# Kernel tuning notes

Hardware: AMD Instinct MI355X
Metric: run time of the kernel (lower is better)

## Reference

```python
import jax, jax.numpy as jnp
import numpy as np

B, T, LD, HD, NH, NL = 8, 16, 256, 512, 8, 6
N = 65           # num_patches + 1 tokens per frame from encoder
AED = 64         # action_embed_dim
NDA = 11         # num_discrete_actions
MLP = 4 * HD


def _ln(x, g, b, eps=1e-5):
    m = jnp.mean(x, -1, keepdims=True)
    v = jnp.mean((x - m) ** 2, -1, keepdims=True)
    return (x - m) / jnp.sqrt(v + eps) * g + b


def setup_inputs() -> dict:
    key = jax.random.key(0)
    ks = iter(jax.random.split(key, 48))
    def nrm(shape):
        return jax.random.normal(next(ks), shape, jnp.float32) * 0.02
    inp = {
        'z_sequence': jax.random.normal(next(ks), (B, T, N, LD), jnp.float32),
        'continuous_actions': jax.random.normal(next(ks), (B, T, 2), jnp.float32),
        'discrete_actions': jax.random.randint(next(ks), (B, T), 0, NDA),
        'w_de': nrm((NDA, AED)),
        'w_cp': nrm((2, AED)), 'b_cp': jnp.zeros((AED,), jnp.float32),
        'w_ap': nrm((2 * AED, HD)), 'b_ap': jnp.zeros((HD,), jnp.float32),
        'w_tp': nrm((LD, HD)), 'b_tp': jnp.zeros((HD,), jnp.float32),
        'w_te': nrm((64, HD)),
        'ln1_g': jnp.ones((NL, HD), jnp.float32), 'ln1_b': jnp.zeros((NL, HD), jnp.float32),
        'wq': nrm((NL, HD, HD)), 'bq': jnp.zeros((NL, HD), jnp.float32),
        'wk': nrm((NL, HD, HD)), 'bk': jnp.zeros((NL, HD), jnp.float32),
        'wv': nrm((NL, HD, HD)), 'bv': jnp.zeros((NL, HD), jnp.float32),
        'wo': nrm((NL, HD, HD)), 'bo': jnp.zeros((NL, HD), jnp.float32),
        'ln2_g': jnp.ones((NL, HD), jnp.float32), 'ln2_b': jnp.zeros((NL, HD), jnp.float32),
        'w1': nrm((NL, HD, MLP)), 'b1': jnp.zeros((NL, MLP), jnp.float32),
        'w2': nrm((NL, MLP, HD)), 'b2': jnp.zeros((NL, HD), jnp.float32),
        'norm_g': jnp.ones((HD,), jnp.float32), 'norm_b': jnp.zeros((HD,), jnp.float32),
        'w_out': nrm((HD, LD)), 'b_out': jnp.zeros((LD,), jnp.float32),
        'residual_weight': jnp.float32(0.5),
    }
    return inp


def reference(z_sequence, continuous_actions, discrete_actions,
              w_de, w_cp, b_cp, w_ap, b_ap, w_tp, b_tp, w_te,
              ln1_g, ln1_b, wq, bq, wk, bk, wv, bv, wo, bo,
              ln2_g, ln2_b, w1, b1, w2, b2,
              norm_g, norm_b, w_out, b_out, residual_weight):
    Bq, Tq, Nq, Dq = z_sequence.shape
    hd = HD // NH
    scale = hd ** -0.5
    # --- per-timestep action + patch token embedding (vectorized over T) ---
    de = w_de[discrete_actions]                          # (B,T,AED)
    ce = continuous_actions @ w_cp + b_cp                # (B,T,AED)
    ac = jnp.concatenate([de, ce], -1)                   # (B,T,2*AED)
    at = (ac @ w_ap + b_ap)[:, :, None, :]               # (B,T,1,HD) action token
    pt = z_sequence @ w_tp + b_tp                        # (B,T,N,HD)
    te = w_te[:Tq][None, :, None, :]                     # (1,T,1,HD) time embedding
    x = jnp.concatenate([at + te, pt + te], axis=2)      # (B,T,1+N,HD) interleaved
    S = Tq * (Nq + 1)
    x = x.reshape(Bq, S, HD)
    # --- block-causal mask: True = cannot attend ---
    ts = jnp.repeat(jnp.arange(Tq), Nq + 1)
    mask = ts[None, :] > ts[:, None]                     # (S,S)

    def body(h, p):
        g1, be1, Wq, Bq_, Wk, Bk_, Wv, Bv_, Wo, Bo_, g2, be2, W1, B1, W2, B2 = p
        y = _ln(h, g1, be1)
        q = (y @ Wq + Bq_).reshape(Bq, S, NH, hd)
        k = (y @ Wk + Bk_).reshape(Bq, S, NH, hd)
        v = (y @ Wv + Bv_).reshape(Bq, S, NH, hd)
        sc = jnp.einsum('bqhd,bkhd->bhqk', q, k) * scale
        sc = jnp.where(mask[None, None], -jnp.inf, sc)
        a = jax.nn.softmax(sc, axis=-1)
        o = jnp.einsum('bhqk,bkhd->bqhd', a, v).reshape(Bq, S, HD)
        h = h + o @ Wo + Bo_
        y = _ln(h, g2, be2)
        h = h + jax.nn.gelu(y @ W1 + B1, approximate=False) @ W2 + B2
        return h, None

    x, _ = jax.lax.scan(body, x, (ln1_g, ln1_b, wq, bq, wk, bk, wv, bv, wo, bo,
                                  ln2_g, ln2_b, w1, b1, w2, b2))
    x = _ln(x, norm_g, norm_b)
    patch_out = x.reshape(Bq, Tq, Nq + 1, HD)[:, :, 1:, :] @ w_out + b_out
    alpha = jax.nn.sigmoid(residual_weight)
    return z_sequence + alpha * patch_out
```

## Files before the change

### kernel.cpp

```cpp
#include <hip/hip_runtime.h>
#include <hip/hip_bf16.h>
#include <cmath>

typedef __attribute__((ext_vector_type(8)))  __bf16 bf16x8;
typedef __attribute__((ext_vector_type(4)))  float  f32x4;
typedef __attribute__((ext_vector_type(16))) float  f32x16;
typedef const __attribute__((address_space(1))) void* as1cv;
typedef __attribute__((address_space(3))) void*       as3v;

static constexpr int BB = 8, TT = 16, NN = 65, LD = 256, HD = 512, NH = 8, NL = 6;
static constexpr int SS    = TT * (NN + 1);
static constexpr int ROWS  = BB * SS;
static constexpr int PROWS = BB * TT * NN;
static constexpr int MLPD  = 2048;

__global__ void transpose_cast(const float* __restrict__ in, __bf16* __restrict__ out,
                               int R, int C, size_t ibs, size_t obs)
{
  __shared__ float t[32][33];
  in  += ibs * blockIdx.z;
  out += obs * blockIdx.z;
  int bx = blockIdx.x * 32, by = blockIdx.y * 32;
  #pragma unroll
  for (int i = threadIdx.y; i < 32; i += 8)
    t[i][threadIdx.x] = in[(size_t)(by + i) * C + bx + threadIdx.x];
  __syncthreads();
  #pragma unroll
  for (int i = threadIdx.y; i < 32; i += 8)
    out[(size_t)(bx + i) * R + by + threadIdx.x] = (__bf16)t[threadIdx.x][i];
}

__global__ __launch_bounds__(256) void cast_bf16(const float* __restrict__ in,
                                                 __bf16* __restrict__ out)
{
  int i = (blockIdx.x * 256 + threadIdx.x) * 8;
  float4 a = *(const float4*)(in + i);
  float4 b = *(const float4*)(in + i + 4);
  bf16x8 o;
  o[0]=(__bf16)a.x; o[1]=(__bf16)a.y; o[2]=(__bf16)a.z; o[3]=(__bf16)a.w;
  o[4]=(__bf16)b.x; o[5]=(__bf16)b.y; o[6]=(__bf16)b.z; o[7]=(__bf16)b.w;
  *(bf16x8*)(out + i) = o;
}

__global__ void build_bqkv(const float* __restrict__ bq, const float* __restrict__ bk,
                           const float* __restrict__ bv, float* __restrict__ out)
{
  int i = blockIdx.x * 256 + threadIdx.x;
  int L = i / 1536, c = i % 1536;
  float v = (c < 512) ? bq[L*512 + c] : (c < 1024 ? bk[L*512 + c - 512] : bv[L*512 + c - 1024]);
  out[i] = v;
}

template<int FLAGS>
__global__ __launch_bounds__(256)
void gemm_bt(const __bf16* __restrict__ A, const __bf16* __restrict__ Bt,
             const float* __restrict__ bias, const float* __restrict__ resid,
             float* __restrict__ outF, __bf16* __restrict__ outB, __bf16* __restrict__ outB2,
             int M, int N, int K)
{
  __shared__ __bf16 As[128 * 64];
  __shared__ __bf16 Bs[128 * 64];
  const int tid = threadIdx.x;
  const int lane = tid & 63, w = tid >> 6;
  const int g = lane >> 4, cl = lane & 15;
  const int wr = w >> 1, wc = w & 1;
  const int tm = blockIdx.y * 128, tn = blockIdx.x * 128;

  f32x4 acc[4][4];
  const f32x4 zero4 = {0.f, 0.f, 0.f, 0.f};
  #pragma unroll
  for (int m = 0; m < 4; m++)
    #pragma unroll
    for (int n = 0; n < 4; n++) acc[m][n] = zero4;

  const int nk = K >> 6;
  for (int kt = 0; kt < nk; ++kt) {
    __syncthreads();
    const __bf16* Ag = A  + (size_t)tm * K + kt * 64;
    const __bf16* Bg = Bt + (size_t)tn * K + kt * 64;
    #pragma unroll
    for (int p = 0; p < 4; p++) {
      int c = p * 256 + tid;
      int row = c >> 3, j = c & 7;
      int jj = j ^ (row & 7);
      const __bf16* sa = Ag + (size_t)row * K + jj * 8;
      const __bf16* sb = Bg + (size_t)row * K + jj * 8;
      __bf16* la = &As[(p * 4 + w) * 512];
      __bf16* lb = &Bs[(p * 4 + w) * 512];
      __builtin_amdgcn_global_load_lds((as1cv)sa, (as3v)la, 16, 0, 0);
      __builtin_amdgcn_global_load_lds((as1cv)sb, (as3v)lb, 16, 0, 0);
    }
    __syncthreads();
    #pragma unroll
    for (int kk = 0; kk < 2; kk++) {
      bf16x8 af[4], bfr[4];
      #pragma unroll
      for (int m = 0; m < 4; m++) {
        int row = wr * 64 + m * 16 + cl;
        int j16 = (kk * 4 + g) ^ (row & 7);
        af[m] = *(const bf16x8*)&As[row * 64 + j16 * 8];
      }
      #pragma unroll
      for (int n = 0; n < 4; n++) {
        int row = wc * 64 + n * 16 + cl;
        int j16 = (kk * 4 + g) ^ (row & 7);
        bfr[n] = *(const bf16x8*)&Bs[row * 64 + j16 * 8];
      }
      #pragma unroll
      for (int m = 0; m < 4; m++)
        #pragma unroll
        for (int n = 0; n < 4; n++)
          acc[m][n] = __builtin_amdgcn_mfma_f32_16x16x32_bf16(af[m], bfr[n], acc[m][n], 0, 0, 0);
    }
  }
  float bv[4];
  #pragma unroll
  for (int n = 0; n < 4; n++) bv[n] = bias[tn + wc * 64 + n * 16 + cl];
  #pragma unroll
  for (int m = 0; m < 4; m++) {
    int Rb = tm + wr * 64 + m * 16 + g * 4;
    #pragma unroll
    for (int i = 0; i < 4; i++) {
      int R = Rb + i;
      #pragma unroll
      for (int n = 0; n < 4; n++) {
        int C = tn + wc * 64 + n * 16 + cl;
        float v = acc[m][n][i] + bv[n];
        if (FLAGS & 1) v = 0.5f * v * (1.f + erff(v * 0.70710678118f));
        if (FLAGS & 2) v += resid[(size_t)R * N + C];
        if (FLAGS & 8) outF[(size_t)R * N + C] = v;
        if (FLAGS & 4) outB[(size_t)R * N + C] = (__bf16)v;
        if (FLAGS & 32) {
          if (C < 1024) {
            outB[(size_t)R * 1024 + C] = (__bf16)v;
          } else {
            int bb2 = R / SS, s2 = R % SS;
            int cc = C - 1024, hh = cc >> 6, dd = cc & 63;
            outB2[((size_t)((bb2 * NH + hh) * 64 + dd)) * SS + s2] = (__bf16)v;
          }
        }
      }
    }
  }
}

__global__ __launch_bounds__(256) void ln_bf16(const float* __restrict__ in,
    const float* __restrict__ gam, const float* __restrict__ bet, __bf16* __restrict__ out)
{
  int w = threadIdx.x >> 6, l = threadIdx.x & 63;
  size_t row = (size_t)blockIdx.x * 4 + w;
  const float4* x4 = (const float4*)(in + row * HD);
  float4 v0 = x4[l], v1 = x4[l + 64];
  float s  = v0.x + v0.y + v0.z + v0.w + v1.x + v1.y + v1.z + v1.w;
  float q2 = v0.x*v0.x + v0.y*v0.y + v0.z*v0.z + v0.w*v0.w
           + v1.x*v1.x + v1.y*v1.y + v1.z*v1.z + v1.w*v1.w;
  #pragma unroll
  for (int m = 1; m < 64; m <<= 1) { s += __shfl_xor(s, m); q2 += __shfl_xor(q2, m); }
  float mean = s * (1.f / HD);
  float rstd = rsqrtf(q2 * (1.f / HD) - mean * mean + 1e-5f);
  int c0 = l * 4, c1 = 256 + l * 4;
  float4 g0 = *(const float4*)(gam + c0), g1 = *(const float4*)(gam + c1);
  float4 e0 = *(const float4*)(bet + c0), e1 = *(const float4*)(bet + c1);
  __bf16* o = out + row * HD;
  o[c0+0] = (__bf16)((v0.x-mean)*rstd*g0.x + e0.x);
  o[c0+1] = (__bf16)((v0.y-mean)*rstd*g0.y + e0.y);
  o[c0+2] = (__bf16)((v0.z-mean)*rstd*g0.z + e0.z);
  o[c0+3] = (__bf16)((v0.w-mean)*rstd*g0.w + e0.w);
  o[c1+0] = (__bf16)((v1.x-mean)*rstd*g1.x + e1.x);
  o[c1+1] = (__bf16)((v1.y-mean)*rstd*g1.y + e1.y);
  o[c1+2] = (__bf16)((v1.z-mean)*rstd*g1.z + e1.z);
  o[c1+3] = (__bf16)((v1.w-mean)*rstd*g1.w + e1.w);
}

__global__ __launch_bounds__(64) void act_embed(const float* __restrict__ cont,
    const int* __restrict__ disc, const float* __restrict__ w_de,
    const float* __restrict__ w_cp, const float* __restrict__ b_cp,
    const float* __restrict__ w_ap, const float* __restrict__ b_ap,
    const float* __restrict__ w_te, float* __restrict__ x)
{
  int t = blockIdx.x, b = blockIdx.y, l = threadIdx.x;
  int da = disc[b * TT + t];
  float c0 = cont[(b * TT + t) * 2], c1 = cont[(b * TT + t) * 2 + 1];
  int c = l * 8;
  float accv[8];
  #pragma unroll
  for (int j = 0; j < 8; j++) accv[j] = b_ap[c + j];
  for (int i = 0; i < 64; i++) {
    float ai = w_de[da * 64 + i];
    #pragma unroll
    for (int j = 0; j < 8; j++) accv[j] += ai * w_ap[i * HD + c + j];
  }
  for (int i = 0; i < 64; i++) {
    float ce = c0 * w_cp[i] + c1 * w_cp[64 + i] + b_cp[i];
    #pragma unroll
    for (int j = 0; j < 8; j++) accv[j] += ce * w_ap[(64 + i) * HD + c + j];
  }
  #pragma unroll
  for (int j = 0; j < 8; j++)
    x[((size_t)(b * SS) + t * 66) * HD + c + j] = accv[j] + w_te[t * HD + c + j];
}

__global__ __launch_bounds__(256) void assemble_patch(const float* __restrict__ pt,
    const float* __restrict__ te, float* __restrict__ x)
{
  int idx = (blockIdx.x * 256 + threadIdx.x) * 4;
  int c = idx & (HD - 1);
  int r = idx >> 9;
  int n = r % NN; int bt = r / NN; int t = bt & (TT - 1); int bb = bt >> 4;
  float4 v  = *(const float4*)(pt + idx);
  float4 tv = *(const float4*)(te + t * HD + c);
  v.x += tv.x; v.y += tv.y; v.z += tv.z; v.w += tv.w;
  *(float4*)(x + ((size_t)(bb * SS + t * 66 + 1 + n)) * HD + c) = v;
}

__device__ inline unsigned pkbf(float lo, float hi2) {
  unsigned short a = __builtin_bit_cast(unsigned short, (__bf16)lo);
  unsigned short b = __builtin_bit_cast(unsigned short, (__bf16)hi2);
  return (unsigned)a | ((unsigned)b << 16);
}

__global__ __launch_bounds__(256) void attn_fwd(const __bf16* __restrict__ qk,
    const __bf16* __restrict__ vT, __bf16* __restrict__ o)
{
  const int w = threadIdx.x >> 6, lane = threadIdx.x & 63;
  const int h = blockIdx.y, b = blockIdx.z;
  int qt;
  if (blockIdx.x == 8) qt = (w == 0) ? 16 : -1;
  else {
    int j = blockIdx.x;
    qt = (w == 0) ? j : (w == 1) ? 32 - j : (w == 2) ? 8 + j : 24 - j;
  }
  __shared__ float red[4][32];
  if (qt < 0) return;
  const int l31 = lane & 31, hi = lane >> 5;
  const int q = qt * 32 + l31;
  const int kend = (q / 66 + 1) * 66;
  const int nkv = (((qt * 32 + 31) / 66 + 1) * 66 + 31) >> 5;

  bf16x8 qf[4];
  const __bf16* qbase = qk + (size_t)(b * SS + q) * 1024 + h * 64 + hi * 8;
  #pragma unroll
  for (int s = 0; s < 4; s++) qf[s] = *(const bf16x8*)(qbase + s * 16);

  const f32x16 z16 = {0,0,0,0,0,0,0,0,0,0,0,0,0,0,0,0};
  f32x16 accA = z16, accB = z16;
  float m = -1e30f, lsum = 0.f;

  for (int kb = 0; kb < nkv; kb++) {
    const int K0 = kb * 32;
    const __bf16* kbase = qk + (size_t)(b * SS + K0 + l31) * 1024 + 512 + h * 64 + hi * 8;
    bf16x8 kf0 = *(const bf16x8*)(kbase);
    bf16x8 kf1 = *(const bf16x8*)(kbase + 16);
    bf16x8 kf2 = *(const bf16x8*)(kbase + 32);
    bf16x8 kf3 = *(const bf16x8*)(kbase + 48);
    const __bf16* vbase = vT + (size_t)((b * NH + h) * 64 + l31) * SS + K0 + hi * 8;
    bf16x8 vf00 = *(const bf16x8*)(vbase);
    bf16x8 vf10 = *(const bf16x8*)(vbase + 16);
    bf16x8 vf01 = *(const bf16x8*)(vbase + (size_t)32 * SS);
    bf16x8 vf11 = *(const bf16x8*)(vbase + (size_t)32 * SS + 16);

    f32x16 st = z16;
    st = __builtin_amdgcn_mfma_f32_32x32x16_bf16(kf0, qf[0], st, 0, 0, 0);
    st = __builtin_amdgcn_mfma_f32_32x32x16_bf16(kf1, qf[1], st, 0, 0, 0);
    st = __builtin_amdgcn_mfma_f32_32x32x16_bf16(kf2, qf[2], st, 0, 0, 0);
    st = __builtin_amdgcn_mfma_f32_32x32x16_bf16(kf3, qf[3], st, 0, 0, 0);

    float p[16];
    #pragma unroll
    for (int r = 0; r < 16; r++) {
      int kg = K0 + (r & 3) + 8 * (r >> 2) + 4 * hi;
      p[r] = (kg < kend) ? st[r] * 0.125f : -1e30f;
    }
    float mx = fmaxf(fmaxf(fmaxf(p[0],p[1]),fmaxf(p[2],p[3])),
                     fmaxf(fmaxf(p[4],p[5]),fmaxf(p[6],p[7])));
    mx = fmaxf(mx, fmaxf(fmaxf(fmaxf(p[8],p[9]),fmaxf(p[10],p[11])),
                         fmaxf(fmaxf(p[12],p[13]),fmaxf(p[14],p[15]))));
    mx = fmaxf(mx, __shfl_xor(mx, 32));
    if (__any(mx > m + 8.f)) {
      float nm = fmaxf(m, mx);
      float alp = __expf(m - nm);
      m = nm; lsum *= alp;
      if (lane < 32) red[w][lane] = alp;
      asm volatile("s_waitcnt lgkmcnt(0)" ::: "memory");
      float4 a0 = *(const float4*)&red[w][hi * 4];
      float4 a1 = *(const float4*)&red[w][hi * 4 + 8];
      float4 a2 = *(const float4*)&red[w][hi * 4 + 16];
      float4 a3 = *(const float4*)&red[w][hi * 4 + 24];
      float afv[16] = {a0.x,a0.y,a0.z,a0.w, a1.x,a1.y,a1.z,a1.w,
                       a2.x,a2.y,a2.z,a2.w, a3.x,a3.y,a3.z,a3.w};
      #pragma unroll
      for (int r = 0; r < 16; r++) { accA[r] *= afv[r]; accB[r] *= afv[r]; }
    }
    float rs;
    #pragma unroll
    for (int r = 0; r < 16; r++) p[r] = __expf(p[r] - m);
    rs = ((p[0]+p[1])+(p[2]+p[3])) + ((p[4]+p[5])+(p[6]+p[7]))
       + ((p[8]+p[9])+(p[10]+p[11])) + ((p[12]+p[13])+(p[14]+p[15]));
    rs += __shfl_xor(rs, 32);
    lsum += rs;
    unsigned a0p = pkbf(p[0], p[1]),  a1p = pkbf(p[2], p[3]);
    unsigned a2p = pkbf(p[4], p[5]),  a3p = pkbf(p[6], p[7]);
    unsigned b0p = pkbf(p[8], p[9]),  b1p = pkbf(p[10], p[11]);
    unsigned b2p = pkbf(p[12], p[13]), b3p = pkbf(p[14], p[15]);
    unsigned s0 = __shfl_xor(a0p, 32), s1 = __shfl_xor(a1p, 32);
    unsigned s2 = __shfl_xor(a2p, 32), s3 = __shfl_xor(a3p, 32);
    unsigned t0 = __shfl_xor(b0p, 32), t1 = __shfl_xor(b1p, 32);
    unsigned t2 = __shfl_xor(b2p, 32), t3 = __shfl_xor(b3p, 32);
    union { unsigned u[4]; bf16x8 v; } af0, af1;
    af0.u[0] = hi ? s2 : a0p;  af0.u[1] = hi ? s3 : a1p;
    af0.u[2] = hi ? a2p : s0;  af0.u[3] = hi ? a3p : s1;
    af1.u[0] = hi ? t2 : b0p;  af1.u[1] = hi ? t3 : b1p;
    af1.u[2] = hi ? b2p : t0;  af1.u[3] = hi ? b3p : t1;
    accA = __builtin_amdgcn_mfma_f32_32x32x16_bf16(af0.v, vf00, accA, 0, 0, 0);
    accA = __builtin_amdgcn_mfma_f32_32x32x16_bf16(af1.v, vf10, accA, 0, 0, 0);
    accB = __builtin_amdgcn_mfma_f32_32x32x16_bf16(af0.v, vf01, accB, 0, 0, 0);
    accB = __builtin_amdgcn_mfma_f32_32x32x16_bf16(af1.v, vf11, accB, 0, 0, 0);
  }
  if (lane < 32) red[w][lane] = 1.f / lsum;
  asm volatile("s_waitcnt lgkmcnt(0)" ::: "memory");
  float4 i0 = *(const float4*)&red[w][hi * 4];
  float4 i1 = *(const float4*)&red[w][hi * 4 + 8];
  float4 i2 = *(const float4*)&red[w][hi * 4 + 16];
  float4 i3 = *(const float4*)&red[w][hi * 4 + 24];
  float iv[16] = {i0.x,i0.y,i0.z,i0.w, i1.x,i1.y,i1.z,i1.w,
                  i2.x,i2.y,i2.z,i2.w, i3.x,i3.y,i3.z,i3.w};
  __bf16* obase = o + (size_t)(b * SS + qt * 32) * HD + h * 64 + l31;
  #pragma unroll
  for (int r = 0; r < 16; r++) {
    int qrow = (r & 3) + 8 * (r >> 2) + 4 * hi;
    obase[(size_t)qrow * HD]      = (__bf16)(accA[r] * iv[r]);
    obase[(size_t)qrow * HD + 32] = (__bf16)(accB[r] * iv[r]);
  }
}

__global__ __launch_bounds__(256) void final_add(const float* __restrict__ z,
    const float* __restrict__ po, const float* __restrict__ rw, float* __restrict__ out)
{
  int idx = (blockIdx.x * 256 + threadIdx.x) * 4;
  int ld = idx & (LD - 1);
  int r = idx >> 8;
  int n = r % NN; int bt = r / NN; int t = bt & (TT - 1); int bb = bt >> 4;
  float alpha = 1.f / (1.f + __expf(-rw[0]));
  float4 zv = *(const float4*)(z + idx);
  float4 pv = *(const float4*)(po + ((size_t)(bb * SS + t * 66 + 1 + n)) * LD + ld);
  float4 ov;
  ov.x = zv.x + alpha * pv.x; ov.y = zv.y + alpha * pv.y;
  ov.z = zv.z + alpha * pv.z; ov.w = zv.w + alpha * pv.w;
  *(float4*)(out + idx) = ov;
}

extern "C" void kernel_launch(void* const* d_in, const int* in_sizes, int n_in,
                              void* d_out, int out_size, void* d_ws, size_t ws_size,
                              hipStream_t stream)
{
  const float* z    = (const float*)d_in[0];
  const float* cont = (const float*)d_in[1];
  const int*   disc = (const int*)d_in[2];
  const float* w_de = (const float*)d_in[3];
  const float* w_cp = (const float*)d_in[4];
  const float* b_cp = (const float*)d_in[5];
  const float* w_ap = (const float*)d_in[6];
  const float* b_ap = (const float*)d_in[7];
  const float* w_tp = (const float*)d_in[8];
  const float* b_tp = (const float*)d_in[9];
  const float* w_te = (const float*)d_in[10];
  const float* ln1g = (const float*)d_in[11];
  const float* ln1b = (const float*)d_in[12];
  const float* wq   = (const float*)d_in[13];
  const float* bq   = (const float*)d_in[14];
  const float* wk   = (const float*)d_in[15];
  const float* bk   = (const float*)d_in[16];
  const float* wv   = (const float*)d_in[17];
  const float* bv   = (const float*)d_in[18];
  const float* wo   = (const float*)d_in[19];
  const float* bo   = (const float*)d_in[20];
  const float* ln2g = (const float*)d_in[21];
  const float* ln2b = (const float*)d_in[22];
  const float* w1   = (const float*)d_in[23];
  const float* b1   = (const float*)d_in[24];
  const float* w2   = (const float*)d_in[25];
  const float* b2   = (const float*)d_in[26];
  const float* nog  = (const float*)d_in[27];
  const float* nob  = (const float*)d_in[28];
  const float* wout = (const float*)d_in[29];
  const float* bout = (const float*)d_in[30];
  const float* rw   = (const float*)d_in[31];
  float* out = (float*)d_out;

  char* p = (char*)d_ws;
  auto alloc = [&](size_t bytes) -> char* {
    char* r = p; p += (bytes + 255) & ~(size_t)255; return r;
  };
  __bf16* wqkvt = (__bf16*)alloc((size_t)NL * 1536 * 512 * 2);
  __bf16* wot_  = (__bf16*)alloc((size_t)NL * 512 * 512 * 2);
  __bf16* w1t   = (__bf16*)alloc((size_t)NL * 512 * 2048 * 2);
  __bf16* w2t   = (__bf16*)alloc((size_t)NL * 512 * 2048 * 2);
  __bf16* wtpt  = (__bf16*)alloc((size_t)512 * 256 * 2);
  __bf16* woutt = (__bf16*)alloc((size_t)256 * 512 * 2);
  float*  bqkv  = (float*)alloc((size_t)NL * 1536 * 4);
  __bf16* zbf   = (__bf16*)alloc((size_t)PROWS * LD * 2);
  float*  x     = (float*)alloc((size_t)ROWS * HD * 4);
  __bf16* y     = (__bf16*)alloc((size_t)ROWS * HD * 2);
  __bf16* qkb   = (__bf16*)alloc((size_t)ROWS * 1024 * 2);
  __bf16* vtb   = (__bf16*)alloc((size_t)ROWS * HD * 2);
  __bf16* ob    = (__bf16*)alloc((size_t)ROWS * HD * 2);
  __bf16* mid   = (__bf16*)alloc((size_t)ROWS * MLPD * 2);
  float*  ptb   = (float*)alloc((size_t)PROWS * HD * 4);
  (void)in_sizes; (void)n_in; (void)out_size; (void)ws_size;

  dim3 tb(32, 8);
  transpose_cast<<<dim3(16, 16, 6), tb, 0, stream>>>(wq, wqkvt,          512,  512,  262144, 786432);
  transpose_cast<<<dim3(16, 16, 6), tb, 0, stream>>>(wk, wqkvt + 262144, 512,  512,  262144, 786432);
  transpose_cast<<<dim3(16, 16, 6), tb, 0, stream>>>(wv, wqkvt + 524288, 512,  512,  262144, 786432);
  transpose_cast<<<dim3(16, 16, 6), tb, 0, stream>>>(wo, wot_,           512,  512,  262144, 262144);
  transpose_cast<<<dim3(64, 16, 6), tb, 0, stream>>>(w1, w1t,            512,  2048, 1048576, 1048576);
  transpose_cast<<<dim3(16, 64, 6), tb, 0, stream>>>(w2, w2t,            2048, 512,  1048576, 1048576);
  transpose_cast<<<dim3(16, 8, 1),  tb, 0, stream>>>(w_tp, wtpt,         256,  512,  0, 0);
  transpose_cast<<<dim3(8, 16, 1),  tb, 0, stream>>>(wout, woutt,        512,  256,  0, 0);
  build_bqkv<<<36, 256, 0, stream>>>(bq, bk, bv, bqkv);
  cast_bf16<<<(PROWS * LD) / 2048, 256, 0, stream>>>(z, zbf);

  gemm_bt<8><<<dim3(4, 65), 256, 0, stream>>>(zbf, wtpt, b_tp, nullptr, ptb, nullptr, nullptr,
                                              PROWS, 512, 256);
  act_embed<<<dim3(16, 8), 64, 0, stream>>>(cont, disc, w_de, w_cp, b_cp, w_ap, b_ap, w_te, x);
  assemble_patch<<<(PROWS * HD) / 1024, 256, 0, stream>>>(ptb, w_te, x);

  for (int L = 0; L < NL; ++L) {
    ln_bf16<<<ROWS / 4, 256, 0, stream>>>(x, ln1g + L*HD, ln1b + L*HD, y);
    gemm_bt<32><<<dim3(12, 66), 256, 0, stream>>>(y, wqkvt + (size_t)L*786432, bqkv + L*1536,
                                                  nullptr, nullptr, qkb, vtb, ROWS, 1536, 512);
    attn_fwd<<<dim3(9, NH, BB), 256, 0, stream>>>(qkb, vtb, ob);
    gemm_bt<10><<<dim3(4, 66), 256, 0, stream>>>(ob, wot_ + (size_t)L*262144, bo + L*HD,
                                                 x, x, nullptr, nullptr, ROWS, 512, 512);
    ln_bf16<<<ROWS / 4, 256, 0, stream>>>(x, ln2g + L*HD, ln2b + L*HD, y);
    gemm_bt<5><<<dim3(16, 66), 256, 0, stream>>>(y, w1t + (size_t)L*1048576, b1 + L*MLPD,
                                                 nullptr, nullptr, mid, nullptr, ROWS, 2048, 512);
    gemm_bt<10><<<dim3(4, 66), 256, 0, stream>>>(mid, w2t + (size_t)L*1048576, b2 + L*HD,
                                                 x, x, nullptr, nullptr, ROWS, 512, 2048);
  }
  ln_bf16<<<ROWS / 4, 256, 0, stream>>>(x, nog, nob, y);
  gemm_bt<8><<<dim3(2, 66), 256, 0, stream>>>(y, woutt, bout, nullptr, ptb, nullptr, nullptr,
                                              ROWS, 256, 512);
  final_add<<<(PROWS * LD) / 1024, 256, 0, stream>>>(z, ptb, rw, out);
}
```

Before: 1.284 ms.

## Add 256x256 double-buffered GEMM kernel for QKV and MLP-up projections

```diff
diff --git a/kernel.cpp b/kernel.cpp
--- a/kernel.cpp
+++ b/kernel.cpp
@@ -7,6 +7,9 @@
 typedef __attribute__((ext_vector_type(16))) float  f32x16;
 typedef const __attribute__((address_space(1))) void* as1cv;
 typedef __attribute__((address_space(3))) void*       as3v;
+
+#define GBAR()  asm volatile("s_barrier" ::: "memory")
+#define VMW(n)  asm volatile("s_waitcnt vmcnt(" #n ")" ::: "memory")
 
 static constexpr int BB = 8, TT = 16, NN = 65, LD = 256, HD = 512, NH = 8, NL = 6;
 static constexpr int SS    = TT * (NN + 1);
@@ -85,10 +88,8 @@
       int jj = j ^ (row & 7);
       const __bf16* sa = Ag + (size_t)row * K + jj * 8;
       const __bf16* sb = Bg + (size_t)row * K + jj * 8;
-      __bf16* la = &As[(p * 4 + w) * 512];
-      __bf16* lb = &Bs[(p * 4 + w) * 512];
-      __builtin_amdgcn_global_load_lds((as1cv)sa, (as3v)la, 16, 0, 0);
-      __builtin_amdgcn_global_load_lds((as1cv)sb, (as3v)lb, 16, 0, 0);
+      __builtin_amdgcn_global_load_lds((as1cv)sa, (as3v)&As[(p * 4 + w) * 512], 16, 0, 0);
+      __builtin_amdgcn_global_load_lds((as1cv)sb, (as3v)&Bs[(p * 4 + w) * 512], 16, 0, 0);
     }
     __syncthreads();
     #pragma unroll
@@ -97,14 +98,12 @@
       #pragma unroll
       for (int m = 0; m < 4; m++) {
         int row = wr * 64 + m * 16 + cl;
-        int j16 = (kk * 4 + g) ^ (row & 7);
-        af[m] = *(const bf16x8*)&As[row * 64 + j16 * 8];
+        af[m] = *(const bf16x8*)&As[row * 64 + ((kk * 4 + g) ^ (row & 7)) * 8];
       }
       #pragma unroll
       for (int n = 0; n < 4; n++) {
         int row = wc * 64 + n * 16 + cl;
-        int j16 = (kk * 4 + g) ^ (row & 7);
-        bfr[n] = *(const bf16x8*)&Bs[row * 64 + j16 * 8];
+        bfr[n] = *(const bf16x8*)&Bs[row * 64 + ((kk * 4 + g) ^ (row & 7)) * 8];
       }
       #pragma unroll
       for (int m = 0; m < 4; m++)
@@ -126,6 +125,139 @@
       for (int n = 0; n < 4; n++) {
         int C = tn + wc * 64 + n * 16 + cl;
         float v = acc[m][n][i] + bv[n];
+        if (FLAGS & 1) v = 0.5f * v * (1.f + erff(v * 0.70710678118f));
+        if (FLAGS & 2) v += resid[(size_t)R * N + C];
+        if (FLAGS & 8) outF[(size_t)R * N + C] = v;
+        if (FLAGS & 4) outB[(size_t)R * N + C] = (__bf16)v;
+        if (FLAGS & 32) {
+          if (C < 1024) {
+            outB[(size_t)R * 1024 + C] = (__bf16)v;
+          } else {
+            int bb2 = R / SS, s2 = R % SS;
+            int cc = C - 1024, hh = cc >> 6, dd = cc & 63;
+            outB2[((size_t)((bb2 * NH + hh) * 64 + dd)) * SS + s2] = (__bf16)v;
+          }
+        }
+      }
+    }
+  }
+}
+
+#define PHASE(BUF, MH, NH, STAGE, VMASM)                                        \
+  {                                                                             \
+    bf16x8 paf[4][2], pbf[2][2];                                                \
+    _Pragma("unroll") for (int mq = 0; mq < 4; mq++)                            \
+      _Pragma("unroll") for (int kk = 0; kk < 2; kk++) {                        \
+        int rl = (MH)*128 + wm*64 + mq*16 + cl;                                 \
+        paf[mq][kk] = *(const bf16x8*)&Al[BUF][rl*64 + (((kk*4+g)^(rl&7))*8)];  \
+      }                                                                         \
+    _Pragma("unroll") for (int nq = 0; nq < 2; nq++)                            \
+      _Pragma("unroll") for (int kk = 0; kk < 2; kk++) {                        \
+        int rl = (NH)*128 + wn*32 + nq*16 + cl;                                 \
+        pbf[nq][kk] = *(const bf16x8*)&Bl[BUF][rl*64 + (((kk*4+g)^(rl&7))*8)];  \
+      }                                                                         \
+    STAGE;                                                                      \
+    GBAR();                                                                     \
+    __builtin_amdgcn_s_setprio(1);                                              \
+    _Pragma("unroll") for (int mq = 0; mq < 4; mq++)                            \
+      _Pragma("unroll") for (int nq = 0; nq < 2; nq++)                          \
+        _Pragma("unroll") for (int kk = 0; kk < 2; kk++)                        \
+          acc[(MH)*4+mq][(NH)*2+nq] = __builtin_amdgcn_mfma_f32_16x16x32_bf16(  \
+              paf[mq][kk], pbf[nq][kk], acc[(MH)*4+mq][(NH)*2+nq], 0, 0, 0);    \
+    __builtin_amdgcn_s_setprio(0);                                              \
+    VMASM;                                                                      \
+    GBAR();                                                                     \
+  }
+
+template<int FLAGS>
+__global__ __launch_bounds__(512, 1)
+void gemm256(const __bf16* __restrict__ A, const __bf16* __restrict__ Bt,
+             const float* __restrict__ bias, const float* __restrict__ resid,
+             float* __restrict__ outF, __bf16* __restrict__ outB, __bf16* __restrict__ outB2,
+             int M, int N, int K)
+{
+  __shared__ __bf16 Al[2][256 * 64];
+  __shared__ __bf16 Bl[2][256 * 64];
+  const int tid = threadIdx.x;
+  const int lane = tid & 63, w = tid >> 6;
+  const int g = lane >> 4, cl = lane & 15;
+  const int wm = w >> 2, wn = w & 3;
+  const int tm = blockIdx.y * 256, tn = blockIdx.x * 256;
+
+  f32x4 acc[8][4];
+  const f32x4 zero4 = {0.f, 0.f, 0.f, 0.f};
+  #pragma unroll
+  for (int m = 0; m < 8; m++)
+    #pragma unroll
+    for (int n = 0; n < 4; n++) acc[m][n] = zero4;
+
+  auto stageA = [&](int buf, int kt, int mh) {
+    #pragma unroll
+    for (int p = 0; p < 2; p++) {
+      int c = p * 512 + tid;
+      int rl = c >> 3, j = c & 7;
+      int jj = j ^ (rl & 7);
+      int srow = p * 128 + mh * 64 + (rl & 63);
+      const __bf16* src = A + (size_t)(tm + srow) * K + kt * 64 + jj * 8;
+      __builtin_amdgcn_global_load_lds((as1cv)src,
+          (as3v)&Al[buf][mh * 8192 + p * 4096 + w * 512], 16, 0, 0);
+    }
+  };
+  auto stageB = [&](int buf, int kt, int nh) {
+    #pragma unroll
+    for (int p = 0; p < 2; p++) {
+      int c = p * 512 + tid;
+      int rl = c >> 3, j = c & 7;
+      int jj = j ^ (rl & 7);
+      int srow = (rl >> 5) * 64 + nh * 32 + (rl & 31);
+      const __bf16* src = Bt + (size_t)(tn + srow) * K + kt * 64 + jj * 8;
+      __builtin_amdgcn_global_load_lds((as1cv)src,
+          (as3v)&Bl[buf][nh * 8192 + p * 4096 + w * 512], 16, 0, 0);
+    }
+  };
+
+  stageA(0, 0, 0); stageB(0, 0, 0); stageB(0, 0, 1); stageA(0, 0, 1);
+  VMW(4);
+  GBAR();
+
+  const int itn = K >> 7;
+  for (int it = 0; it < itn - 1; ++it) {
+    const int ta = 2 * it + 1, tb = 2 * it + 2;
+    PHASE(0, 0, 0, { stageA(1, ta, 0); }, VMW(4));
+    PHASE(0, 0, 1, { stageB(1, ta, 0); }, VMW(4));
+    PHASE(0, 1, 0, { stageB(1, ta, 1); }, VMW(4));
+    PHASE(0, 1, 1, { stageA(1, ta, 1); }, VMW(4));
+    PHASE(1, 0, 0, { stageA(0, tb, 0); }, VMW(4));
+    PHASE(1, 0, 1, { stageB(0, tb, 0); }, VMW(4));
+    PHASE(1, 1, 0, { stageB(0, tb, 1); }, VMW(4));
+    PHASE(1, 1, 1, { stageA(0, tb, 1); }, VMW(4));
+  }
+  {
+    const int ta = (K >> 6) - 1;
+    PHASE(0, 0, 0, { stageA(1, ta, 0); }, VMW(4));
+    PHASE(0, 0, 1, { stageB(1, ta, 0); }, VMW(4));
+    PHASE(0, 1, 0, { stageB(1, ta, 1); }, VMW(4));
+    PHASE(0, 1, 1, { stageA(1, ta, 1); }, VMW(4));
+    PHASE(1, 0, 0, { }, VMW(2));
+    PHASE(1, 0, 1, { }, VMW(0));
+    PHASE(1, 1, 0, { }, (void)0);
+    PHASE(1, 1, 1, { }, (void)0);
+  }
+
+  float bv[4];
+  #pragma unroll
+  for (int nn = 0; nn < 4; nn++)
+    bv[nn] = bias[tn + wn * 64 + (nn >> 1) * 32 + (nn & 1) * 16 + cl];
+  #pragma unroll
+  for (int mm = 0; mm < 8; mm++) {
+    int Rb = tm + wm * 128 + (mm >> 2) * 64 + (mm & 3) * 16 + g * 4;
+    #pragma unroll
+    for (int i = 0; i < 4; i++) {
+      int R = Rb + i;
+      #pragma unroll
+      for (int nn = 0; nn < 4; nn++) {
+        int C = tn + wn * 64 + (nn >> 1) * 32 + (nn & 1) * 16 + cl;
+        float v = acc[mm][nn][i] + bv[nn];
         if (FLAGS & 1) v = 0.5f * v * (1.f + erff(v * 0.70710678118f));
         if (FLAGS & 2) v += resid[(size_t)R * N + C];
         if (FLAGS & 8) outF[(size_t)R * N + C] = v;
@@ -427,14 +559,14 @@
 
   for (int L = 0; L < NL; ++L) {
     ln_bf16<<<ROWS / 4, 256, 0, stream>>>(x, ln1g + L*HD, ln1b + L*HD, y);
-    gemm_bt<32><<<dim3(12, 66), 256, 0, stream>>>(y, wqkvt + (size_t)L*786432, bqkv + L*1536,
-                                                  nullptr, nullptr, qkb, vtb, ROWS, 1536, 512);
+    gemm256<32><<<dim3(6, 33), 512, 0, stream>>>(y, wqkvt + (size_t)L*786432, bqkv + L*1536,
+                                                 nullptr, nullptr, qkb, vtb, ROWS, 1536, 512);
     attn_fwd<<<dim3(9, NH, BB), 256, 0, stream>>>(qkb, vtb, ob);
     gemm_bt<10><<<dim3(4, 66), 256, 0, stream>>>(ob, wot_ + (size_t)L*262144, bo + L*HD,
                                                  x, x, nullptr, nullptr, ROWS, 512, 512);
     ln_bf16<<<ROWS / 4, 256, 0, stream>>>(x, ln2g + L*HD, ln2b + L*HD, y);
-    gemm_bt<5><<<dim3(16, 66), 256, 0, stream>>>(y, w1t + (size_t)L*1048576, b1 + L*MLPD,
-                                                 nullptr, nullptr, mid, nullptr, ROWS, 2048, 512);
+    gemm256<5><<<dim3(8, 33), 512, 0, stream>>>(y, w1t + (size_t)L*1048576, b1 + L*MLPD,
+                                                nullptr, nullptr, mid, nullptr, ROWS, 2048, 512);
     gemm_bt<10><<<dim3(4, 66), 256, 0, stream>>>(mid, w2t + (size_t)L*1048576, b2 + L*HD,
                                                  x, x, nullptr, nullptr, ROWS, 512, 2048);
   }
```

Measured after the change: 1.767 ms. 1.38x slower.

## Stage K/V tiles in LDS with double buffering in attention kernel

Applied to the files above, without the earlier changes.

```diff
diff --git a/kernel.cpp b/kernel.cpp
--- a/kernel.cpp
+++ b/kernel.cpp
@@ -7,6 +7,9 @@
 typedef __attribute__((ext_vector_type(16))) float  f32x16;
 typedef const __attribute__((address_space(1))) void* as1cv;
 typedef __attribute__((address_space(3))) void*       as3v;
+
+#define GBAR()  asm volatile("s_barrier" ::: "memory")
+#define VMW0()  asm volatile("s_waitcnt vmcnt(0)" ::: "memory")
 
 static constexpr int BB = 8, TT = 16, NN = 65, LD = 256, HD = 512, NH = 8, NL = 6;
 static constexpr int SS    = TT * (NN + 1);
@@ -85,10 +88,8 @@
       int jj = j ^ (row & 7);
       const __bf16* sa = Ag + (size_t)row * K + jj * 8;
       const __bf16* sb = Bg + (size_t)row * K + jj * 8;
-      __bf16* la = &As[(p * 4 + w) * 512];
-      __bf16* lb = &Bs[(p * 4 + w) * 512];
-      __builtin_amdgcn_global_load_lds((as1cv)sa, (as3v)la, 16, 0, 0);
-      __builtin_amdgcn_global_load_lds((as1cv)sb, (as3v)lb, 16, 0, 0);
+      __builtin_amdgcn_global_load_lds((as1cv)sa, (as3v)&As[(p * 4 + w) * 512], 16, 0, 0);
+      __builtin_amdgcn_global_load_lds((as1cv)sb, (as3v)&Bs[(p * 4 + w) * 512], 16, 0, 0);
     }
     __syncthreads();
     #pragma unroll
@@ -97,14 +98,12 @@
       #pragma unroll
       for (int m = 0; m < 4; m++) {
         int row = wr * 64 + m * 16 + cl;
-        int j16 = (kk * 4 + g) ^ (row & 7);
-        af[m] = *(const bf16x8*)&As[row * 64 + j16 * 8];
+        af[m] = *(const bf16x8*)&As[row * 64 + ((kk * 4 + g) ^ (row & 7)) * 8];
       }
       #pragma unroll
       for (int n = 0; n < 4; n++) {
         int row = wc * 64 + n * 16 + cl;
-        int j16 = (kk * 4 + g) ^ (row & 7);
-        bfr[n] = *(const bf16x8*)&Bs[row * 64 + j16 * 8];
+        bfr[n] = *(const bf16x8*)&Bs[row * 64 + ((kk * 4 + g) ^ (row & 7)) * 8];
       }
       #pragma unroll
       for (int m = 0; m < 4; m++)
@@ -222,20 +221,22 @@
 __global__ __launch_bounds__(256) void attn_fwd(const __bf16* __restrict__ qk,
     const __bf16* __restrict__ vT, __bf16* __restrict__ o)
 {
-  const int w = threadIdx.x >> 6, lane = threadIdx.x & 63;
+  const int tid = threadIdx.x;
+  const int w = tid >> 6, lane = tid & 63;
   const int h = blockIdx.y, b = blockIdx.z;
-  int qt;
-  if (blockIdx.x == 8) qt = (w == 0) ? 16 : -1;
-  else {
-    int j = blockIdx.x;
-    qt = (w == 0) ? j : (w == 1) ? 32 - j : (w == 2) ? 8 + j : 24 - j;
-  }
+  const int l31 = lane & 31, hi = lane >> 5;
+  const int qt = blockIdx.x * 4 + w;
+  const bool qv = qt <= 32;
+  const int q = qv ? qt * 32 + l31 : 0;
+  const int kend = (q / 66 + 1) * 66;
+
+  __shared__ __attribute__((aligned(16))) __bf16 Ks[2][64][64];
+  __shared__ __attribute__((aligned(16))) __bf16 Vs[2][64][64];
   __shared__ float red[4][32];
-  if (qt < 0) return;
-  const int l31 = lane & 31, hi = lane >> 5;
-  const int q = qt * 32 + l31;
-  const int kend = (q / 66 + 1) * 66;
-  const int nkv = (((qt * 32 + 31) / 66 + 1) * 66 + 31) >> 5;
+
+  const int qtmax = min(blockIdx.x * 4 + 3, 32);
+  const int nkv_b = (((qtmax * 32 + 31) / 66 + 1) * 66 + 63) >> 6;
+  const int nkv_w = qv ? ((((qt * 32 + 31) / 66 + 1) * 66 + 63) >> 6) : 0;
 
   bf16x8 qf[4];
   const __bf16* qbase = qk + (size_t)(b * SS + q) * 1024 + h * 64 + hi * 8;
@@ -246,90 +247,150 @@
   f32x16 accA = z16, accB = z16;
   float m = -1e30f, lsum = 0.f;
 
-  for (int kb = 0; kb < nkv; kb++) {
-    const int K0 = kb * 32;
-    const __bf16* kbase = qk + (size_t)(b * SS + K0 + l31) * 1024 + 512 + h * 64 + hi * 8;
-    bf16x8 kf0 = *(const bf16x8*)(kbase);
-    bf16x8 kf1 = *(const bf16x8*)(kbase + 16);
-    bf16x8 kf2 = *(const bf16x8*)(kbase + 32);
-    bf16x8 kf3 = *(const bf16x8*)(kbase + 48);
-    const __bf16* vbase = vT + (size_t)((b * NH + h) * 64 + l31) * SS + K0 + hi * 8;
-    bf16x8 vf00 = *(const bf16x8*)(vbase);
-    bf16x8 vf10 = *(const bf16x8*)(vbase + 16);
-    bf16x8 vf01 = *(const bf16x8*)(vbase + (size_t)32 * SS);
-    bf16x8 vf11 = *(const bf16x8*)(vbase + (size_t)32 * SS + 16);
-
-    f32x16 st = z16;
-    st = __builtin_amdgcn_mfma_f32_32x32x16_bf16(kf0, qf[0], st, 0, 0, 0);
-    st = __builtin_amdgcn_mfma_f32_32x32x16_bf16(kf1, qf[1], st, 0, 0, 0);
-    st = __builtin_amdgcn_mfma_f32_32x32x16_bf16(kf2, qf[2], st, 0, 0, 0);
-    st = __builtin_amdgcn_mfma_f32_32x32x16_bf16(kf3, qf[3], st, 0, 0, 0);
-
-    float p[16];
+  auto stage = [&](int buf, int kb) {
+    const int K0 = kb * 64;
+    #pragma unroll
+    for (int p2 = 0; p2 < 2; p2++) {
+      int c = p2 * 256 + tid;
+      int row = c >> 3, j = c & 7;
+      int jj = j ^ (row & 7);
+      const __bf16* sk = qk + (size_t)(b * SS + min(K0 + row, SS - 1)) * 1024 + 512
+                            + h * 64 + jj * 8;
+      __builtin_amdgcn_global_load_lds((as1cv)sk,
+          (as3v)(&Ks[buf][0][0] + (p2 * 4 + w) * 512), 16, 0, 0);
+      const __bf16* sv = vT + (size_t)((b * NH + h) * 64 + row) * SS
+                            + min(K0 + jj * 8, SS - 8);
+      __builtin_amdgcn_global_load_lds((as1cv)sv,
+          (as3v)(&Vs[buf][0][0] + (p2 * 4 + w) * 512), 16, 0, 0);
+    }
+  };
+
+  stage(0, 0);
+  VMW0();
+  GBAR();
+
+  int buf = 0;
+  for (int kb = 0; kb < nkv_b; ++kb) {
+    if (kb + 1 < nkv_b) stage(buf ^ 1, kb + 1);
+    if (qv && kb < nkv_w) {
+      const int K0 = kb * 64;
+      bf16x8 kfa[4], kfb[4], vfa[4], vfb[4];
+      #pragma unroll
+      for (int s = 0; s < 4; s++) {
+        int ch = ((s * 2 + hi) ^ (l31 & 7)) * 8;
+        kfa[s] = *(const bf16x8*)&Ks[buf][l31][ch];
+        kfb[s] = *(const bf16x8*)&Ks[buf][32 + l31][ch];
+        vfa[s] = *(const bf16x8*)&Vs[buf][l31][ch];
+        vfb[s] = *(const bf16x8*)&Vs[buf][32 + l31][ch];
+      }
+      f32x16 st0 = z16, st1 = z16;
+      st0 = __builtin_amdgcn_mfma_f32_32x32x16_bf16(kfa[0], qf[0], st0, 0, 0, 0);
+      st0 = __builtin_amdgcn_mfma_f32_32x32x16_bf16(kfa[1], qf[1], st0, 0, 0, 0);
+      st0 = __builtin_amdgcn_mfma_f32_32x32x16_bf16(kfa[2], qf[2], st0, 0, 0, 0);
+      st0 = __builtin_amdgcn_mfma_f32_32x32x16_bf16(kfa[3], qf[3], st0, 0, 0, 0);
+      st1 = __builtin_amdgcn_mfma_f32_32x32x16_bf16(kfb[0], qf[0], st1, 0, 0, 0);
+      st1 = __builtin_amdgcn_mfma_f32_32x32x16_bf16(kfb[1], qf[1], st1, 0, 0, 0);
+      st1 = __builtin_amdgcn_mfma_f32_32x32x16_bf16(kfb[2], qf[2], st1, 0, 0, 0);
+      st1 = __builtin_amdgcn_mfma_f32_32x32x16_bf16(kfb[3], qf[3], st1, 0, 0, 0);
+
+      float p0[16], p1[16];
+      #pragma unroll
+      for (int r = 0; r < 16; r++) {
+        int cr = (r & 3) + 8 * (r >> 2) + 4 * hi;
+        p0[r] = (K0 + cr < kend)      ? st0[r] * 0.125f : -1e30f;
+        p1[r] = (K0 + 32 + cr < kend) ? st1[r] * 0.125f : -1e30f;
+      }
+      float mx = fmaxf(fmaxf(fmaxf(p0[0],p0[1]),fmaxf(p0[2],p0[3])),
+                       fmaxf(fmaxf(p0[4],p0[5]),fmaxf(p0[6],p0[7])));
+      mx = fmaxf(mx, fmaxf(fmaxf(fmaxf(p0[8],p0[9]),fmaxf(p0[10],p0[11])),
+                           fmaxf(fmaxf(p0[12],p0[13]),fmaxf(p0[14],p0[15]))));
+      mx = fmaxf(mx, fmaxf(fmaxf(fmaxf(p1[0],p1[1]),fmaxf(p1[2],p1[3])),
+                           fmaxf(fmaxf(p1[4],p1[5]),fmaxf(p1[6],p1[7]))));
+      mx = fmaxf(mx, fmaxf(fmaxf(fmaxf(p1[8],p1[9]),fmaxf(p1[10],p1[11])),
+                           fmaxf(fmaxf(p1[12],p1[13]),fmaxf(p1[14],p1[15]))));
+      mx = fmaxf(mx, __shfl_xor(mx, 32));
+      if (__any(mx > m + 8.f)) {
+        float nm = fmaxf(m, mx);
+        float alp = __expf(m - nm);
+        m = nm; lsum *= alp;
+        if (lane < 32) red[w][lane] = alp;
+        asm volatile("s_waitcnt lgkmcnt(0)" ::: "memory");
+        float4 a0 = *(const float4*)&red[w][hi * 4];
+        float4 a1 = *(const float4*)&red[w][hi * 4 + 8];
+        float4 a2 = *(const float4*)&red[w][hi * 4 + 16];
+        float4 a3 = *(const float4*)&red[w][hi * 4 + 24];
+        float afv[16] = {a0.x,a0.y,a0.z,a0.w, a1.x,a1.y,a1.z,a1.w,
+                         a2.x,a2.y,a2.z,a2.w, a3.x,a3.y,a3.z,a3.w};
+        #pragma unroll
+        for (int r = 0; r < 16; r++) { accA[r] *= afv[r]; accB[r] *= afv[r]; }
+      }
+      #pragma unroll
+      for (int r = 0; r < 16; r++) { p0[r] = __expf(p0[r] - m); p1[r] = __expf(p1[r] - m); }
+      float rs = (((p0[0]+p0[1])+(p0[2]+p0[3])) + ((p0[4]+p0[5])+(p0[6]+p0[7])))
+               + (((p0[8]+p0[9])+(p0[10]+p0[11])) + ((p0[12]+p0[13])+(p0[14]+p0[15])))
+               + (((p1[0]+p1[1])+(p1[2]+p1[3])) + ((p1[4]+p1[5])+(p1[6]+p1[7])))
+               + (((p1[8]+p1[9])+(p1[10]+p1[11])) + ((p1[12]+p1[13])+(p1[14]+p1[15])));
+      rs += __shfl_xor(rs, 32);
+      lsum += rs;
+      union { unsigned u[4]; bf16x8 v; } af00, af10, af01, af11;
+      {
+        unsigned a0p = pkbf(p0[0], p0[1]),  a1p = pkbf(p0[2], p0[3]);
+        unsigned a2p = pkbf(p0[4], p0[5]),  a3p = pkbf(p0[6], p0[7]);
+        unsigned b0p = pkbf(p0[8], p0[9]),  b1p = pkbf(p0[10], p0[11]);
+        unsigned b2p = pkbf(p0[12], p0[13]), b3p = pkbf(p0[14], p0[15]);
+        unsigned s0 = __shfl_xor(a0p, 32), s1 = __shfl_xor(a1p, 32);
+        unsigned s2 = __shfl_xor(a2p, 32), s3 = __shfl_xor(a3p, 32);
+        unsigned t0 = __shfl_xor(b0p, 32), t1 = __shfl_xor(b1p, 32);
+        unsigned t2 = __shfl_xor(b2p, 32), t3 = __shfl_xor(b3p, 32);
+        af00.u[0] = hi ? s2 : a0p;  af00.u[1] = hi ? s3 : a1p;
+        af00.u[2] = hi ? a2p : s0;  af00.u[3] = hi ? a3p : s1;
+        af10.u[0] = hi ? t2 : b0p;  af10.u[1] = hi ? t3 : b1p;
+        af10.u[2] = hi ? b2p : t0;  af10.u[3] = hi ? b3p : t1;
+      }
+      {
+        unsigned a0p = pkbf(p1[0], p1[1]),  a1p = pkbf(p1[2], p1[3]);
+        unsigned a2p = pkbf(p1[4], p1[5]),  a3p = pkbf(p1[6], p1[7]);
+        unsigned b0p = pkbf(p1[8], p1[9]),  b1p = pkbf(p1[10], p1[11]);
+        unsigned b2p = pkbf(p1[12], p1[13]), b3p = pkbf(p1[14], p1[15]);
+        unsigned s0 = __shfl_xor(a0p, 32), s1 = __shfl_xor(a1p, 32);
+        unsigned s2 = __shfl_xor(a2p, 32), s3 = __shfl_xor(a3p, 32);
+        unsigned t0 = __shfl_xor(b0p, 32), t1 = __shfl_xor(b1p, 32);
+        unsigned t2 = __shfl_xor(b2p, 32), t3 = __shfl_xor(b3p, 32);
+        af01.u[0] = hi ? s2 : a0p;  af01.u[1] = hi ? s3 : a1p;
+        af01.u[2] = hi ? a2p : s0;  af01.u[3] = hi ? a3p : s1;
+        af11.u[0] = hi ? t2 : b0p;  af11.u[1] = hi ? t3 : b1p;
+        af11.u[2] = hi ? b2p : t0;  af11.u[3] = hi ? b3p : t1;
+      }
+      accA = __builtin_amdgcn_mfma_f32_32x32x16_bf16(af00.v, vfa[0], accA, 0, 0, 0);
+      accA = __builtin_amdgcn_mfma_f32_32x32x16_bf16(af10.v, vfa[1], accA, 0, 0, 0);
+      accA = __builtin_amdgcn_mfma_f32_32x32x16_bf16(af01.v, vfa[2], accA, 0, 0, 0);
+      accA = __builtin_amdgcn_mfma_f32_32x32x16_bf16(af11.v, vfa[3], accA, 0, 0, 0);
+      accB = __builtin_amdgcn_mfma_f32_32x32x16_bf16(af00.v, vfb[0], accB, 0, 0, 0);
+      accB = __builtin_amdgcn_mfma_f32_32x32x16_bf16(af10.v, vfb[1], accB, 0, 0, 0);
+      accB = __builtin_amdgcn_mfma_f32_32x32x16_bf16(af01.v, vfb[2], accB, 0, 0, 0);
+      accB = __builtin_amdgcn_mfma_f32_32x32x16_bf16(af11.v, vfb[3], accB, 0, 0, 0);
+    }
+    VMW0();
+    GBAR();
+    buf ^= 1;
+  }
+
+  if (qv) {
+    if (lane < 32) red[w][lane] = 1.f / lsum;
+    asm volatile("s_waitcnt lgkmcnt(0)" ::: "memory");
+    float4 i0 = *(const float4*)&red[w][hi * 4];
+    float4 i1 = *(const float4*)&red[w][hi * 4 + 8];
+    float4 i2 = *(const float4*)&red[w][hi * 4 + 16];
+    float4 i3 = *(const float4*)&red[w][hi * 4 + 24];
+    float iv[16] = {i0.x,i0.y,i0.z,i0.w, i1.x,i1.y,i1.z,i1.w,
+                    i2.x,i2.y,i2.z,i2.w, i3.x,i3.y,i3.z,i3.w};
+    __bf16* obase = o + (size_t)(b * SS + qt * 32) * HD + h * 64 + l31;
     #pragma unroll
     for (int r = 0; r < 16; r++) {
-      int kg = K0 + (r & 3) + 8 * (r >> 2) + 4 * hi;
-      p[r] = (kg < kend) ? st[r] * 0.125f : -1e30f;
+      int qrow = (r & 3) + 8 * (r >> 2) + 4 * hi;
+      obase[(size_t)qrow * HD]      = (__bf16)(accA[r] * iv[r]);
+      obase[(size_t)qrow * HD + 32] = (__bf16)(accB[r] * iv[r]);
     }
-    float mx = fmaxf(fmaxf(fmaxf(p[0],p[1]),fmaxf(p[2],p[3])),
-                     fmaxf(fmaxf(p[4],p[5]),fmaxf(p[6],p[7])));
-    mx = fmaxf(mx, fmaxf(fmaxf(fmaxf(p[8],p[9]),fmaxf(p[10],p[11])),
-                         fmaxf(fmaxf(p[12],p[13]),fmaxf(p[14],p[15]))));
-    mx = fmaxf(mx, __shfl_xor(mx, 32));
-    if (__any(mx > m + 8.f)) {
-      float nm = fmaxf(m, mx);
-      float alp = __expf(m - nm);
-      m = nm; lsum *= alp;
-      if (lane < 32) red[w][lane] = alp;
-      asm volatile("s_waitcnt lgkmcnt(0)" ::: "memory");
-      float4 a0 = *(const float4*)&red[w][hi * 4];
-      float4 a1 = *(const float4*)&red[w][hi * 4 + 8];
-      float4 a2 = *(const float4*)&red[w][hi * 4 + 16];
-      float4 a3 = *(const float4*)&red[w][hi * 4 + 24];
-      float afv[16] = {a0.x,a0.y,a0.z,a0.w, a1.x,a1.y,a1.z,a1.w,
-                       a2.x,a2.y,a2.z,a2.w, a3.x,a3.y,a3.z,a3.w};
-      #pragma unroll
-      for (int r = 0; r < 16; r++) { accA[r] *= afv[r]; accB[r] *= afv[r]; }
-    }
-    float rs;
-    #pragma unroll
-    for (int r = 0; r < 16; r++) p[r] = __expf(p[r] - m);
-    rs = ((p[0]+p[1])+(p[2]+p[3])) + ((p[4]+p[5])+(p[6]+p[7]))
-       + ((p[8]+p[9])+(p[10]+p[11])) + ((p[12]+p[13])+(p[14]+p[15]));
-    rs += __shfl_xor(rs, 32);
-    lsum += rs;
-    unsigned a0p = pkbf(p[0], p[1]),  a1p = pkbf(p[2], p[3]);
-    unsigned a2p = pkbf(p[4], p[5]),  a3p = pkbf(p[6], p[7]);
-    unsigned b0p = pkbf(p[8], p[9]),  b1p = pkbf(p[10], p[11]);
-    unsigned b2p = pkbf(p[12], p[13]), b3p = pkbf(p[14], p[15]);
-    unsigned s0 = __shfl_xor(a0p, 32), s1 = __shfl_xor(a1p, 32);
-    unsigned s2 = __shfl_xor(a2p, 32), s3 = __shfl_xor(a3p, 32);
-    unsigned t0 = __shfl_xor(b0p, 32), t1 = __shfl_xor(b1p, 32);
-    unsigned t2 = __shfl_xor(b2p, 32), t3 = __shfl_xor(b3p, 32);
-    union { unsigned u[4]; bf16x8 v; } af0, af1;
-    af0.u[0] = hi ? s2 : a0p;  af0.u[1] = hi ? s3 : a1p;
-    af0.u[2] = hi ? a2p : s0;  af0.u[3] = hi ? a3p : s1;
-    af1.u[0] = hi ? t2 : b0p;  af1.u[1] = hi ? t3 : b1p;
-    af1.u[2] = hi ? b2p : t0;  af1.u[3] = hi ? b3p : t1;
-    accA = __builtin_amdgcn_mfma_f32_32x32x16_bf16(af0.v, vf00, accA, 0, 0, 0);
-    accA = __builtin_amdgcn_mfma_f32_32x32x16_bf16(af1.v, vf10, accA, 0, 0, 0);
-    accB = __builtin_amdgcn_mfma_f32_32x32x16_bf16(af0.v, vf01, accB, 0, 0, 0);
-    accB = __builtin_amdgcn_mfma_f32_32x32x16_bf16(af1.v, vf11, accB, 0, 0, 0);
-  }
-  if (lane < 32) red[w][lane] = 1.f / lsum;
-  asm volatile("s_waitcnt lgkmcnt(0)" ::: "memory");
-  float4 i0 = *(const float4*)&red[w][hi * 4];
-  float4 i1 = *(const float4*)&red[w][hi * 4 + 8];
-  float4 i2 = *(const float4*)&red[w][hi * 4 + 16];
-  float4 i3 = *(const float4*)&red[w][hi * 4 + 24];
-  float iv[16] = {i0.x,i0.y,i0.z,i0.w, i1.x,i1.y,i1.z,i1.w,
-                  i2.x,i2.y,i2.z,i2.w, i3.x,i3.y,i3.z,i3.w};
-  __bf16* obase = o + (size_t)(b * SS + qt * 32) * HD + h * 64 + l31;
-  #pragma unroll
-  for (int r = 0; r < 16; r++) {
-    int qrow = (r & 3) + 8 * (r >> 2) + 4 * hi;
-    obase[(size_t)qrow * HD]      = (__bf16)(accA[r] * iv[r]);
-    obase[(size_t)qrow * HD + 32] = (__bf16)(accB[r] * iv[r]);
   }
 }
 
```

After: 1.274 ms. About the same (-0.8%).
